# Performance work log

Hardware: AMD Instinct MI355X
Metric: run time of the kernel (lower is better)

## Reference

```python
import jax, jax.numpy as jnp
import numpy as np

C, H, W = 32, 64, 64
KH, KW = 5, 5
OH, OW = 60, 60
N_IN = C * H * W
B, S = 64, 4096
CAP = 128


def _build_indices():
    # Enumerate every (c, kh, kw, oh, ow) slot of the unfold, matching
    # fold(unfold(order)) in the torch module (stride 1, pad 0, dilation 1).
    c = np.arange(C)[:, None, None, None, None]
    kh = np.arange(KH)[None, :, None, None, None]
    kw = np.arange(KW)[None, None, :, None, None]
    oh = np.arange(OH)[None, None, None, :, None]
    ow = np.arange(OW)[None, None, None, None, :]
    ids = c * (H * W) + (oh + kh) * W + (ow + kw)          # input flat id feeding slot
    ckk = c * (KH * KW) + kh * KW + kw                     # kernel-local channel index
    j = ckk * (OH * OW) + oh * OW + ow                     # flat slot in order_convoled
    ids, j = np.broadcast_arrays(ids, j)
    ids = ids.ravel().astype(np.int64)
    j = j.ravel().astype(np.int64)
    perm = np.argsort(ids, kind='stable')
    sid, sj = ids[perm], j[perm]
    counts = np.bincount(ids, minlength=N_IN)
    Lmax = int(counts.max())                               # = 25 here
    starts = np.concatenate([[0], np.cumsum(counts)[:-1]])
    rank = np.arange(sid.shape[0]) - starts[sid]
    indices = np.full((N_IN, Lmax), -1, dtype=np.int32)
    indices[sid, rank] = sj
    return indices


def setup_inputs() -> dict:
    key = jax.random.key(0)
    spikes = jax.random.randint(key, (B, S, 1, 1), 0, N_IN, dtype=jnp.int32)
    indices = jnp.asarray(_build_indices())
    return {"spikes": spikes, "indices": indices, "out_h": OH, "out_w": OW, "cap": CAP}


def reference(spikes, indices, out_h, out_w, cap):
    Bn, Sn = spikes.shape[0], spikes.shape[1]
    L = indices.shape[1]
    nbins = out_h * out_w
    E = Sn * L                                             # events per batch element

    ids = spikes[:, :, 0, 0]                               # [B,S] flat input ids
    g = indices[ids]                                       # [B,S,L] slots, -1 padded
    valid = g >= 0
    j = jnp.where(valid, g, 0)
    bins = (j % nbins).reshape(Bn * E)                     # output bin (oh*out_w+ow)
    ckk = (j // nbins).reshape(Bn * E)                     # kernel-local index to store
    valid_f = valid.reshape(Bn * E)
    b_idx = jnp.repeat(jnp.arange(Bn, dtype=jnp.int32), E)

    # Arrival-order rank within each (batch, bin): stable sort by global bin,
    # then rank = position - segment start (running max of change points).
    gbin = jnp.where(valid_f, b_idx * nbins + bins, Bn * nbins)   # sentinel for invalid
    perm = jnp.argsort(gbin)                               # stable
    sorted_gbin = gbin[perm]
    pos = jnp.arange(Bn * E, dtype=jnp.int32)
    change = jnp.concatenate([jnp.ones((1,), bool), sorted_gbin[1:] != sorted_gbin[:-1]])
    seg_start = jax.lax.cummax(jnp.where(change, pos, 0))
    rank_sorted = pos - seg_start
    rank = jnp.zeros(Bn * E, jnp.int32).at[perm].set(rank_sorted)  # inverse perm

    # Scatter ckk into per-bin slots; invalid / overflow events go to slot=cap (dropped).
    slot = jnp.where(valid_f & (rank < cap), rank, cap)
    out = jnp.full((Bn, cap + 1, nbins), -1, dtype=spikes.dtype)
    out = out.at[b_idx, slot, bins].set(jnp.where(valid_f, ckk, -1), mode='drop')
    return out[:, :cap].reshape(Bn, cap, out_h, out_w)
```

## Files before the change

### kernel.cpp

```cpp
#include <hip/hip_runtime.h>

#define OHh   60
#define OWw   60
#define NBINS (OHh * OWw)
#define NB    64
#define NS    4096
#define CAP   128

#define NW     4
#define RPB    2
#define RG     (OHh / RPB)
#define SEGS   2
#define SEG    (NS / SEGS)
#define CH     (SEG / 64)
#define WSLOTS 40
#define PRE0   64

__global__ __launch_bounds__(256) void sort_spikes_rowpair(
    const int* __restrict__ spikes, int* __restrict__ out) {
    const int bid  = (int)blockIdx.x;
    const int b    = bid & (NB - 1);
    const int rg   = bid >> 6;
    const int tid  = (int)threadIdx.x;
    const int wv   = tid >> 6;
    const int lane = tid & 63;
    const bool valid  = lane < OWw;
    const int  lane_c = valid ? lane : 127;

    const int rsub = wv >> 1;
    const int seg  = wv & 1;
    const int row  = rg * RPB + rsub;

    __shared__ short          stage[NW][WSLOTS + 1][64];
    __shared__ unsigned short hits[NW][64];
    __shared__ int            cnt[NW][64];
    __shared__ int            ovf;

    if (tid == 0) ovf = 0;

    const int* __restrict__ sp   = spikes + b * NS + seg * SEG;
    int* __restrict__       outb = out + (size_t)b * (CAP * NBINS) + row * OWw;

    unsigned short* const hitbuf      = &hits[wv][0];
    short* const          stage_lane  = &stage[wv][0][lane];
    short* const          stage_dummy = &stage[wv][WSLOTS][lane];

    int count = 0;
#pragma unroll
    for (int half = 0; half < 2; ++half) {
        int vs[16];
#pragma unroll
        for (int c = 0; c < 16; ++c) vs[c] = sp[(half * 16 + c) * 64 + lane];

#pragma unroll
        for (int c = 0; c < 16; ++c) {
            const int cc  = half * 16 + c;
            const int v   = vs[c];
            const int kh  = ((v >> 6) & 63) - row;
            const bool halo = (unsigned)kh < 5u;
            const int w   = v & 63;
            const int A   = (v >> 12) * 25 + kh * 5 + w;
            const unsigned short P = (unsigned short)((w << 10) | A);

            const unsigned long long mask = __ballot(halo);
            const int pos = __builtin_amdgcn_mbcnt_hi(
                (unsigned)(mask >> 32),
                __builtin_amdgcn_mbcnt_lo((unsigned)mask, 0));
            if (halo) hitbuf[pos] = P;
            const int n = __popcll(mask);

            for (int i = 0; i < n; ++i) {
                const int Pj  = (int)hitbuf[i];
                const int kw  = (Pj >> 10) - lane_c;
                const bool inwin = (unsigned)kw < 5u;
                const int val = (Pj & 0x3ff) - lane_c;
                short* a = (inwin & (count < WSLOTS))
                               ? (stage_lane + count * 64)
                               : stage_dummy;
                *a = (short)val;
                count += inwin;
            }

            if (valid) outb[(PRE0 + seg * CH + cc) * NBINS + lane] = -1;
        }
    }
    cnt[wv][lane] = count;
    if (__ballot(count > WSLOTS) && lane == 0) ovf = 1;
    __syncthreads();

    if (ovf == 0) {
        if (valid) {
            const int w0 = rsub * SEGS;
            const int c0 = cnt[w0][lane], c1 = cnt[w0 + 1][lane];
            const int total = c0 + c1;
            const int kbase = seg * 32;
#pragma unroll 4
            for (int i = 0; i < 32; ++i) {
                const int k = kbase + i;
                int val = -1;
                if (k < total) {
                    const int wsel = (k >= c0) ? (w0 + 1) : w0;
                    const int base = (k >= c0) ? c0 : 0;
                    val = (int)stage[wsel][k - base][lane];
                }
                outb[k * NBINS + lane] = val;
            }
            for (int k = PRE0 + seg; k < total && k < CAP; k += SEGS) {
                const int wsel = (k >= c0) ? (w0 + 1) : w0;
                const int base = (k >= c0) ? c0 : 0;
                outb[k * NBINS + lane] = (int)stage[wsel][k - base][lane];
            }
        }
    } else if (seg == 0) {
        const int* __restrict__ spf = spikes + b * NS;
        int cc = 0;
        for (int c = 0; c < NS / 64; ++c) {
            const int v = spf[c * 64 + lane];
            const int h = (v >> 6) & 63;
            unsigned long long mask = __ballot((unsigned)(h - row) < 5u);
            while (mask) {
                const int j = (int)__builtin_ctzll(mask);
                mask &= mask - 1;
                const int vj =
                    __builtin_amdgcn_readlane(v, __builtin_amdgcn_readfirstlane(j));
                const int wj  = vj & 63;
                const int khj = ((vj >> 6) & 63) - row;
                const int cj  = vj >> 12;
                const int kw  = wj - lane;
                if (((unsigned)kw < 5u) & valid) {
                    if (cc < CAP)
                        outb[cc * NBINS + lane] = cj * 25 + khj * 5 + kw;
                    ++cc;
                }
            }
        }
        if (valid)
            for (int k = cc; k < CAP; ++k) outb[k * NBINS + lane] = -1;
    }
}

extern "C" void kernel_launch(void* const* d_in, const int* in_sizes, int n_in,
                              void* d_out, int out_size, void* d_ws, size_t ws_size,
                              hipStream_t stream) {
    const int* spikes = (const int*)d_in[0];
    int* out = (int*)d_out;

    dim3 grid(RG * NB);
    dim3 block(256);
    sort_spikes_rowpair<<<grid, block, 0, stream>>>(spikes, out);
}
```

Before: 153.6 us.

## Split spike stream into four segments and process four rows per block

Each block now covers four output rows with 16 waves, and every row's spike stream is split across four waves instead of two. This shortens each wave's serial ballot/scan loop and halves the grid size. It also lowers per-wave staging slots from 40 to 32 and merges staged hits across four segments when writing out. The smaller slot count makes the slow serial overflow fallback more likely, and the 1024-thread blocks with larger shared memory may reduce occupancy.

```diff
diff --git a/kernel.cpp b/kernel.cpp
--- a/kernel.cpp
+++ b/kernel.cpp
@@ -7,16 +7,16 @@
 #define NS    4096
 #define CAP   128
 
-#define NW     4
-#define RPB    2
+#define NW     16
+#define RPB    4
 #define RG     (OHh / RPB)
-#define SEGS   2
+#define SEGS   4
 #define SEG    (NS / SEGS)
 #define CH     (SEG / 64)
-#define WSLOTS 40
+#define WSLOTS 32
 #define PRE0   64
 
-__global__ __launch_bounds__(256) void sort_spikes_rowpair(
+__global__ __launch_bounds__(1024) void sort_spikes_row4x(
     const int* __restrict__ spikes, int* __restrict__ out) {
     const int bid  = (int)blockIdx.x;
     const int b    = bid & (NB - 1);
@@ -27,8 +27,8 @@
     const bool valid  = lane < OWw;
     const int  lane_c = valid ? lane : 127;
 
-    const int rsub = wv >> 1;
-    const int seg  = wv & 1;
+    const int rsub = wv >> 2;
+    const int seg  = wv & 3;
     const int row  = rg * RPB + rsub;
 
     __shared__ short          stage[NW][WSLOTS + 1][64];
@@ -41,48 +41,44 @@
     const int* __restrict__ sp   = spikes + b * NS + seg * SEG;
     int* __restrict__       outb = out + (size_t)b * (CAP * NBINS) + row * OWw;
 
+    int vs[CH];
+#pragma unroll
+    for (int c = 0; c < CH; ++c) vs[c] = sp[c * 64 + lane];
+
     unsigned short* const hitbuf      = &hits[wv][0];
     short* const          stage_lane  = &stage[wv][0][lane];
     short* const          stage_dummy = &stage[wv][WSLOTS][lane];
 
     int count = 0;
 #pragma unroll
-    for (int half = 0; half < 2; ++half) {
-        int vs[16];
-#pragma unroll
-        for (int c = 0; c < 16; ++c) vs[c] = sp[(half * 16 + c) * 64 + lane];
+    for (int c = 0; c < CH; ++c) {
+        const int v   = vs[c];
+        const int kh  = ((v >> 6) & 63) - row;
+        const bool halo = (unsigned)kh < 5u;
+        const int w   = v & 63;
+        const int A   = (v >> 12) * 25 + kh * 5 + w;
+        const unsigned short P = (unsigned short)((w << 10) | A);
 
-#pragma unroll
-        for (int c = 0; c < 16; ++c) {
-            const int cc  = half * 16 + c;
-            const int v   = vs[c];
-            const int kh  = ((v >> 6) & 63) - row;
-            const bool halo = (unsigned)kh < 5u;
-            const int w   = v & 63;
-            const int A   = (v >> 12) * 25 + kh * 5 + w;
-            const unsigned short P = (unsigned short)((w << 10) | A);
+        const unsigned long long mask = __ballot(halo);
+        const int pos = __builtin_amdgcn_mbcnt_hi(
+            (unsigned)(mask >> 32),
+            __builtin_amdgcn_mbcnt_lo((unsigned)mask, 0));
+        if (halo) hitbuf[pos] = P;
+        const int n = __popcll(mask);
 
-            const unsigned long long mask = __ballot(halo);
-            const int pos = __builtin_amdgcn_mbcnt_hi(
-                (unsigned)(mask >> 32),
-                __builtin_amdgcn_mbcnt_lo((unsigned)mask, 0));
-            if (halo) hitbuf[pos] = P;
-            const int n = __popcll(mask);
+        for (int i = 0; i < n; ++i) {
+            const int Pj  = (int)hitbuf[i];
+            const int kw  = (Pj >> 10) - lane_c;
+            const bool inwin = (unsigned)kw < 5u;
+            const int val = (Pj & 0x3ff) - lane_c;
+            short* a = (inwin & (count < WSLOTS))
+                           ? (stage_lane + count * 64)
+                           : stage_dummy;
+            *a = (short)val;
+            count += inwin;
+        }
 
-            for (int i = 0; i < n; ++i) {
-                const int Pj  = (int)hitbuf[i];
-                const int kw  = (Pj >> 10) - lane_c;
-                const bool inwin = (unsigned)kw < 5u;
-                const int val = (Pj & 0x3ff) - lane_c;
-                short* a = (inwin & (count < WSLOTS))
-                               ? (stage_lane + count * 64)
-                               : stage_dummy;
-                *a = (short)val;
-                count += inwin;
-            }
-
-            if (valid) outb[(PRE0 + seg * CH + cc) * NBINS + lane] = -1;
-        }
+        if (valid) outb[(PRE0 + seg * CH + c) * NBINS + lane] = -1;
     }
     cnt[wv][lane] = count;
     if (__ballot(count > WSLOTS) && lane == 0) ovf = 1;
@@ -92,22 +88,27 @@
         if (valid) {
             const int w0 = rsub * SEGS;
             const int c0 = cnt[w0][lane], c1 = cnt[w0 + 1][lane];
-            const int total = c0 + c1;
-            const int kbase = seg * 32;
+            const int c2 = cnt[w0 + 2][lane], c3 = cnt[w0 + 3][lane];
+            const int o1 = c0, o2 = c0 + c1, o3 = o2 + c2;
+            const int total = o3 + c3;
 #pragma unroll 4
-            for (int i = 0; i < 32; ++i) {
-                const int k = kbase + i;
+            for (int i = 0; i < PRE0 / SEGS; ++i) {
+                const int k = seg * (PRE0 / SEGS) + i;
                 int val = -1;
                 if (k < total) {
-                    const int wsel = (k >= c0) ? (w0 + 1) : w0;
-                    const int base = (k >= c0) ? c0 : 0;
+                    int wsel = w0, base = 0;
+                    if (k >= o1) { wsel = w0 + 1; base = o1; }
+                    if (k >= o2) { wsel = w0 + 2; base = o2; }
+                    if (k >= o3) { wsel = w0 + 3; base = o3; }
                     val = (int)stage[wsel][k - base][lane];
                 }
                 outb[k * NBINS + lane] = val;
             }
             for (int k = PRE0 + seg; k < total && k < CAP; k += SEGS) {
-                const int wsel = (k >= c0) ? (w0 + 1) : w0;
-                const int base = (k >= c0) ? c0 : 0;
+                int wsel = w0, base = 0;
+                if (k >= o1) { wsel = w0 + 1; base = o1; }
+                if (k >= o2) { wsel = w0 + 2; base = o2; }
+                if (k >= o3) { wsel = w0 + 3; base = o3; }
                 outb[k * NBINS + lane] = (int)stage[wsel][k - base][lane];
             }
         }
@@ -146,6 +147,6 @@
     int* out = (int*)d_out;
 
     dim3 grid(RG * NB);
-    dim3 block(256);
-    sort_spikes_rowpair<<<grid, block, 0, stream>>>(spikes, out);
+    dim3 block(NW * 64);
+    sort_spikes_row4x<<<grid, block, 0, stream>>>(spikes, out);
 }
```

Result: no change. 153.5 us (-0.0%).
